# Performance work log

Hardware: AMD Instinct MI355X
Metric: run time of the kernel (lower is better)

Reference implementation:

```python
import jax, jax.numpy as jnp
import numpy as np

N = 50000      # nodes
E = 800000     # edges (before self-loops)
IN = 256       # in_channels
HID = 64       # hidden_channels per head
HEADS = 8
OUT = 64       # out_channels
NEG_SLOPE = 0.2  # PyG GATConv leaky_relu slope


def gat_conv(x, W, a_src, a_dst, b, src, dst, heads, outc, concat):
    # x: [n, f_in]; W: [f_in, heads*outc]; a_src/a_dst: [heads, outc]; b: bias
    n = x.shape[0]
    h = (x @ W).reshape(n, heads, outc)                      # [n, H, C]
    alpha_s = (h * a_src).sum(-1)                            # [n, H]
    alpha_d = (h * a_dst).sum(-1)                            # [n, H]
    e = jax.nn.leaky_relu(alpha_s[src] + alpha_d[dst], NEG_SLOPE)  # [E, H]
    # segment softmax over destination node
    m = jax.lax.stop_gradient(jax.ops.segment_max(e, dst, num_segments=n))
    ex = jnp.exp(e - m[dst])                                 # [E, H]
    den = jax.ops.segment_sum(ex, dst, num_segments=n)       # [n, H]
    alpha = ex / (den[dst] + 1e-16)                          # [E, H]
    out = jax.ops.segment_sum(alpha[..., None] * h[src], dst, num_segments=n)  # [n, H, C]
    out = out.reshape(n, heads * outc) if concat else out.mean(axis=1)
    return out + b


def setup_inputs() -> dict:
    key = jax.random.key(0)
    ks = jax.random.split(key, 10)
    s = 0.1
    return {
        "x": jax.random.normal(ks[0], (N, IN), jnp.float32),
        "edge_index": jax.random.randint(ks[1], (2, E), 0, N, dtype=jnp.int64)
            if jax.config.jax_enable_x64 else jax.random.randint(ks[1], (2, E), 0, N, dtype=jnp.int32),
        "W1": jax.random.normal(ks[2], (IN, HEADS * HID), jnp.float32) * s,
        "a_src1": jax.random.normal(ks[3], (HEADS, HID), jnp.float32) * s,
        "a_dst1": jax.random.normal(ks[4], (HEADS, HID), jnp.float32) * s,
        "b1": jnp.zeros((HEADS * HID,), jnp.float32),
        "W2": jax.random.normal(ks[5], (HEADS * HID, OUT), jnp.float32) * s,
        "a_src2": jax.random.normal(ks[6], (1, OUT), jnp.float32) * s,
        "a_dst2": jax.random.normal(ks[7], (1, OUT), jnp.float32) * s,
        "b2": jnp.zeros((OUT,), jnp.float32),
    }


def reference(x, W1, a_src1, a_dst1, b1, W2, a_src2, a_dst2, b2, edge_index):
    # eval mode: dropout is identity. PyG GATConv adds self-loops by default.
    loop = jnp.arange(N, dtype=edge_index.dtype)
    src = jnp.concatenate([edge_index[0], loop])
    dst = jnp.concatenate([edge_index[1], loop])
    h = jax.nn.elu(gat_conv(x, W1, a_src1, a_dst1, b1, src, dst, HEADS, HID, True))
    return gat_conv(h, W2, a_src2, a_dst2, b2, src, dst, 1, OUT, False)
```

## Files before the change

### kernel.cpp

```cpp
#include <hip/hip_runtime.h>
#include <cstddef>

#define NN   50000
#define EE   800000
#define TOTE 850000
#define INC  256
#define HEADS 8
#define F1   512
#define OUTC 64
#define NB   ((NN + 255) / 256)

#define PB_CVTX   ((NN * INC / 8 + 255) / 256)
#define PB_CVTW1  ((INC * F1 + 255) / 256)
#define PB_CVTW2  ((F1 * OUTC + 255) / 256)
#define PB_COUNT  ((TOTE + 255) / 256)

typedef unsigned short ushort_t;
typedef unsigned int uint_t;
typedef __attribute__((ext_vector_type(8))) short short8;
typedef __attribute__((ext_vector_type(4))) float f32x4;

__device__ __forceinline__ ushort_t f32_to_bf16_rne(float f) {
  uint_t u = __float_as_uint(f);
  u += 0x7fffu + ((u >> 16) & 1u);
  return (ushort_t)(u >> 16);
}
__device__ __forceinline__ float bf16lo_to_f32(uint_t u) {
  return __uint_as_float(u << 16);
}
__device__ __forceinline__ float bf16hi_to_f32(uint_t u) {
  return __uint_as_float(u & 0xffff0000u);
}
__device__ __forceinline__ float lrelu(float x) { return fmaxf(x, 0.2f * x); }

__device__ __forceinline__ void gload16(const ushort_t* g, ushort_t* l) {
  __builtin_amdgcn_global_load_lds(
      (const __attribute__((address_space(1))) void*)g,
      (__attribute__((address_space(3))) void*)l, 16, 0, 0);
}

__global__ __launch_bounds__(256)
void prelude_kernel(const float* __restrict__ x, ushort_t* __restrict__ xbf,
                    const float* __restrict__ W1, ushort_t* __restrict__ W1T,
                    const float* __restrict__ W2, ushort_t* __restrict__ W2T,
                    const int* __restrict__ dsts, int* __restrict__ deg) {
  int b = blockIdx.x;
  if (b < PB_CVTX) {
    long i = ((long)b * 256 + threadIdx.x) * 8;
    if (i >= (long)NN * INC) return;
    float4 v0 = *reinterpret_cast<const float4*>(x + i);
    float4 v1 = *reinterpret_cast<const float4*>(x + i + 4);
    ushort_t p[8] = {f32_to_bf16_rne(v0.x), f32_to_bf16_rne(v0.y),
                     f32_to_bf16_rne(v0.z), f32_to_bf16_rne(v0.w),
                     f32_to_bf16_rne(v1.x), f32_to_bf16_rne(v1.y),
                     f32_to_bf16_rne(v1.z), f32_to_bf16_rne(v1.w)};
    *reinterpret_cast<uint4*>(xbf + i) = *reinterpret_cast<uint4*>(p);
    return;
  }
  b -= PB_CVTX;
  if (b < PB_CVTW1) {
    int i = b * 256 + threadIdx.x;
    if (i >= INC * F1) return;
    int k = i / F1, n = i % F1;
    W1T[(size_t)n * INC + k] = f32_to_bf16_rne(W1[i]);
    return;
  }
  b -= PB_CVTW1;
  if (b < PB_CVTW2) {
    int i = b * 256 + threadIdx.x;
    if (i >= F1 * OUTC) return;
    int k = i / OUTC, n = i % OUTC;
    W2T[(size_t)n * F1 + k] = f32_to_bf16_rne(W2[i]);
    return;
  }
  b -= PB_CVTW2;
  {
    int e = b * 256 + threadIdx.x;
    if (e >= TOTE) return;
    int dst = (e < EE) ? dsts[e] : (e - EE);
    atomicAdd(&deg[dst], 1);
  }
}

__global__ __launch_bounds__(256, 2)
void gemm_mfma(const ushort_t* __restrict__ A, const ushort_t* __restrict__ BT,
               const float* __restrict__ a_src, const float* __restrict__ a_dst,
               ushort_t* __restrict__ Cbf, float* __restrict__ AS,
               float* __restrict__ AD, int M, int K, int Nn, int nheads) {
  __shared__ __align__(16) ushort_t sA[128 * 64];
  __shared__ __align__(16) ushort_t sB[64 * 64];
  const int tid = threadIdx.x;
  const int w = tid >> 6, lane = tid & 63;

  int p = blockIdx.x;
  int nwg = gridDim.x;
  int l = ((nwg & 7) == 0) ? ((p & 7) * (nwg >> 3) + (p >> 3)) : p;
  const int rowBase = (l / nheads) * 128;
  const int head = l % nheads;
  const int colBase = head * 64;

  const int l8 = lane >> 3;
  const int srcslot = (lane & 7) ^ l8;
  size_t aOff[4]; ushort_t* aLds[4];
  #pragma unroll
  for (int q = 0; q < 4; ++q) {
    int r0 = w * 32 + q * 8;
    int grow = rowBase + r0 + l8; if (grow > M - 1) grow = M - 1;
    aOff[q] = (size_t)grow * K + srcslot * 8;
    aLds[q] = sA + r0 * 64;
  }
  size_t bOff[2]; ushort_t* bLds[2];
  #pragma unroll
  for (int q = 0; q < 2; ++q) {
    int c0 = w * 16 + q * 8;
    bOff[q] = (size_t)(colBase + c0 + l8) * K + srcslot * 8;
    bLds[q] = sB + c0 * 64;
  }

  f32x4 acc[2][4];
  #pragma unroll
  for (int mf = 0; mf < 2; ++mf)
    #pragma unroll
    for (int cf = 0; cf < 4; ++cf)
      acc[mf][cf] = (f32x4){0.f, 0.f, 0.f, 0.f};

  const int nkt = K >> 6;
  for (int kt = 0; kt < nkt; ++kt) {
    __syncthreads();
    #pragma unroll
    for (int q = 0; q < 4; ++q) gload16(A + aOff[q] + kt * 64, aLds[q]);
    #pragma unroll
    for (int q = 0; q < 2; ++q) gload16(BT + bOff[q] + kt * 64, bLds[q]);
    __syncthreads();
    #pragma unroll
    for (int ks = 0; ks < 2; ++ks) {
      const int sl = ks * 4 + (lane >> 4);
      short8 af[2], bfr[4];
      #pragma unroll
      for (int mf = 0; mf < 2; ++mf) {
        int row = w * 32 + mf * 16 + (lane & 15);
        af[mf] = *reinterpret_cast<short8*>((char*)sA + row * 128 + ((sl ^ (row & 7)) << 4));
      }
      #pragma unroll
      for (int cf = 0; cf < 4; ++cf) {
        int col = cf * 16 + (lane & 15);
        bfr[cf] = *reinterpret_cast<short8*>((char*)sB + col * 128 + ((sl ^ (col & 7)) << 4));
      }
      #pragma unroll
      for (int mf = 0; mf < 2; ++mf)
        #pragma unroll
        for (int cf = 0; cf < 4; ++cf)
          acc[mf][cf] = __builtin_amdgcn_mfma_f32_16x16x32_bf16(af[mf], bfr[cf], acc[mf][cf], 0, 0, 0);
    }
  }

  const int g = lane >> 4, c = lane & 15;
  float asv[4], adv[4];
  #pragma unroll
  for (int cf = 0; cf < 4; ++cf) {
    asv[cf] = a_src[colBase + cf * 16 + c];
    adv[cf] = a_dst[colBase + cf * 16 + c];
  }
  #pragma unroll
  for (int mf = 0; mf < 2; ++mf) {
    #pragma unroll
    for (int r = 0; r < 4; ++r) {
      int row = rowBase + w * 32 + mf * 16 + g * 4 + r;
      bool ok = row < M;
      float s = 0.f, d = 0.f;
      #pragma unroll
      for (int cf = 0; cf < 4; ++cf) {
        float v = acc[mf][cf][r];
        s = fmaf(v, asv[cf], s);
        d = fmaf(v, adv[cf], d);
        if (ok) Cbf[(size_t)row * Nn + colBase + cf * 16 + c] = f32_to_bf16_rne(v);
      }
      #pragma unroll
      for (int off = 8; off > 0; off >>= 1) {
        s += __shfl_xor(s, off);
        d += __shfl_xor(d, off);
      }
      if (ok && c == 0) {
        AS[(size_t)row * nheads + head] = s;
        AD[(size_t)row * nheads + head] = d;
      }
    }
  }
}

__global__ __launch_bounds__(256)
void scanA_kernel(const int* __restrict__ deg, int* __restrict__ rowptr,
                  int* __restrict__ psum) {
  __shared__ int sh[256];
  int t = threadIdx.x;
  int i = blockIdx.x * 256 + t;
  int v = (i < NN) ? deg[i] : 0;
  sh[t] = v;
  __syncthreads();
  #pragma unroll
  for (int off = 1; off < 256; off <<= 1) {
    int t2 = (t >= off) ? sh[t - off] : 0;
    __syncthreads();
    sh[t] += t2;
    __syncthreads();
  }
  if (i < NN) rowptr[i + 1] = sh[t];
  if (t == 255) psum[blockIdx.x] = sh[255];
}

__global__ __launch_bounds__(256)
void scanC_kernel(int* __restrict__ rowptr, const int* __restrict__ psum) {
  __shared__ int sh[256];
  int t = threadIdx.x;
  int v = (t < NB) ? psum[t] : 0;
  sh[t] = v;
  __syncthreads();
  #pragma unroll
  for (int off = 1; off < 256; off <<= 1) {
    int t2 = (t >= off) ? sh[t - off] : 0;
    __syncthreads();
    sh[t] += t2;
    __syncthreads();
  }
  int base = (blockIdx.x > 0) ? sh[blockIdx.x - 1] : 0;
  int i = blockIdx.x * 256 + t;
  if (i < NN) rowptr[i + 1] += base;
  if (i == 0) rowptr[0] = 0;
}

__global__ __launch_bounds__(256)
void scatter_kernel(const int* __restrict__ srcs, const int* __restrict__ dsts,
                    const int* __restrict__ rowptr, int* __restrict__ cursor,
                    int* __restrict__ esrc) {
  int e = blockIdx.x * blockDim.x + threadIdx.x;
  if (e >= TOTE) return;
  int src, dst;
  if (e < EE) { src = srcs[e]; dst = dsts[e]; }
  else        { src = e - EE;  dst = e - EE; }
  int pos = rowptr[dst] + atomicAdd(&cursor[dst], 1);
  esrc[pos] = src;
}

__global__ __launch_bounds__(256)
void agg1_kernel(const ushort_t* __restrict__ H1bf, const float* __restrict__ AS,
                 const float* __restrict__ AD, const int* __restrict__ rowptr,
                 const int* __restrict__ esrc, const float* __restrict__ b1,
                 ushort_t* __restrict__ OUT) {
  int n = (blockIdx.x * blockDim.x + threadIdx.x) >> 6;
  int lane = threadIdx.x & 63;
  if (n >= NN) return;
  int off = lane * 8;
  int h = lane >> 3;
  float ad = AD[n * HEADS + h];
  int s0 = rowptr[n], s1 = rowptr[n + 1];
  float den = 0.f;
  float a0 = 0.f, a1 = 0.f, a2 = 0.f, a3 = 0.f, a4 = 0.f, a5 = 0.f, a6 = 0.f, a7 = 0.f;
  int j = s0;
  for (; j + 3 < s1; j += 4) {
    int src[4];
    #pragma unroll
    for (int u = 0; u < 4; ++u) src[u] = esrc[j + u];
    float as[4]; uint4 v[4];
    #pragma unroll
    for (int u = 0; u < 4; ++u) {
      as[u] = AS[src[u] * HEADS + h];
      v[u] = *reinterpret_cast<const uint4*>(H1bf + (size_t)src[u] * F1 + off);
    }
    #pragma unroll
    for (int u = 0; u < 4; ++u) {
      float wgt = __expf(lrelu(as[u] + ad));
      den += wgt;
      a0 = fmaf(wgt, bf16lo_to_f32(v[u].x), a0);
      a1 = fmaf(wgt, bf16hi_to_f32(v[u].x), a1);
      a2 = fmaf(wgt, bf16lo_to_f32(v[u].y), a2);
      a3 = fmaf(wgt, bf16hi_to_f32(v[u].y), a3);
      a4 = fmaf(wgt, bf16lo_to_f32(v[u].z), a4);
      a5 = fmaf(wgt, bf16hi_to_f32(v[u].z), a5);
      a6 = fmaf(wgt, bf16lo_to_f32(v[u].w), a6);
      a7 = fmaf(wgt, bf16hi_to_f32(v[u].w), a7);
    }
  }
  for (; j < s1; ++j) {
    int src = esrc[j];
    float as = AS[src * HEADS + h];
    uint4 v = *reinterpret_cast<const uint4*>(H1bf + (size_t)src * F1 + off);
    float wgt = __expf(lrelu(as + ad));
    den += wgt;
    a0 = fmaf(wgt, bf16lo_to_f32(v.x), a0);
    a1 = fmaf(wgt, bf16hi_to_f32(v.x), a1);
    a2 = fmaf(wgt, bf16lo_to_f32(v.y), a2);
    a3 = fmaf(wgt, bf16hi_to_f32(v.y), a3);
    a4 = fmaf(wgt, bf16lo_to_f32(v.z), a4);
    a5 = fmaf(wgt, bf16hi_to_f32(v.z), a5);
    a6 = fmaf(wgt, bf16lo_to_f32(v.w), a6);
    a7 = fmaf(wgt, bf16hi_to_f32(v.w), a7);
  }
  float rden = 1.f / (den + 1e-16f);
  float4 b_lo = *reinterpret_cast<const float4*>(b1 + off);
  float4 b_hi = *reinterpret_cast<const float4*>(b1 + off + 4);
  float r[8];
  r[0] = fmaf(a0, rden, b_lo.x); r[1] = fmaf(a1, rden, b_lo.y);
  r[2] = fmaf(a2, rden, b_lo.z); r[3] = fmaf(a3, rden, b_lo.w);
  r[4] = fmaf(a4, rden, b_hi.x); r[5] = fmaf(a5, rden, b_hi.y);
  r[6] = fmaf(a6, rden, b_hi.z); r[7] = fmaf(a7, rden, b_hi.w);
  ushort_t pk[8];
  #pragma unroll
  for (int i = 0; i < 8; ++i) {
    float e = r[i] > 0.f ? r[i] : expm1f(r[i]);
    pk[i] = f32_to_bf16_rne(e);
  }
  *reinterpret_cast<uint4*>(OUT + (size_t)n * F1 + off) = *reinterpret_cast<uint4*>(pk);
}

__global__ __launch_bounds__(256)
void agg2_kernel(const ushort_t* __restrict__ H2bf, const float* __restrict__ AS,
                 const float* __restrict__ AD, const int* __restrict__ rowptr,
                 const int* __restrict__ esrc, const float* __restrict__ b2,
                 float* __restrict__ OUT) {
  int n = (blockIdx.x * blockDim.x + threadIdx.x) >> 6;
  int lane = threadIdx.x & 63;
  if (n >= NN) return;
  int grp = lane >> 3;
  int c8 = (lane & 7) * 8;
  float ad = AD[n];
  int s0 = rowptr[n], s1 = rowptr[n + 1];
  float den = 0.f;
  float a0 = 0.f, a1 = 0.f, a2 = 0.f, a3 = 0.f, a4 = 0.f, a5 = 0.f, a6 = 0.f, a7 = 0.f;
  for (int j0 = s0; j0 < s1; j0 += 8) {
    int j = j0 + grp;
    bool valid = j < s1;
    int src = esrc[valid ? j : s0];
    float as = AS[src];
    uint4 v = *reinterpret_cast<const uint4*>(H2bf + (size_t)src * OUTC + c8);
    float w = valid ? __expf(lrelu(as + ad)) : 0.f;
    den += w;
    a0 = fmaf(w, bf16lo_to_f32(v.x), a0);
    a1 = fmaf(w, bf16hi_to_f32(v.x), a1);
    a2 = fmaf(w, bf16lo_to_f32(v.y), a2);
    a3 = fmaf(w, bf16hi_to_f32(v.y), a3);
    a4 = fmaf(w, bf16lo_to_f32(v.z), a4);
    a5 = fmaf(w, bf16hi_to_f32(v.z), a5);
    a6 = fmaf(w, bf16lo_to_f32(v.w), a6);
    a7 = fmaf(w, bf16hi_to_f32(v.w), a7);
  }
  #pragma unroll
  for (int st = 8; st < 64; st <<= 1) {
    den += __shfl_xor(den, st);
    a0 += __shfl_xor(a0, st); a1 += __shfl_xor(a1, st);
    a2 += __shfl_xor(a2, st); a3 += __shfl_xor(a3, st);
    a4 += __shfl_xor(a4, st); a5 += __shfl_xor(a5, st);
    a6 += __shfl_xor(a6, st); a7 += __shfl_xor(a7, st);
  }
  if (grp == 0) {
    float rden = 1.f / (den + 1e-16f);
    float4 o0, o1;
    o0.x = fmaf(a0, rden, b2[c8 + 0]); o0.y = fmaf(a1, rden, b2[c8 + 1]);
    o0.z = fmaf(a2, rden, b2[c8 + 2]); o0.w = fmaf(a3, rden, b2[c8 + 3]);
    o1.x = fmaf(a4, rden, b2[c8 + 4]); o1.y = fmaf(a5, rden, b2[c8 + 5]);
    o1.z = fmaf(a6, rden, b2[c8 + 6]); o1.w = fmaf(a7, rden, b2[c8 + 7]);
    *reinterpret_cast<float4*>(OUT + (size_t)n * OUTC + c8) = o0;
    *reinterpret_cast<float4*>(OUT + (size_t)n * OUTC + c8 + 4) = o1;
  }
}

extern "C" void kernel_launch(void* const* d_in, const int* in_sizes, int n_in,
                              void* d_out, int out_size, void* d_ws, size_t ws_size,
                              hipStream_t stream) {
  const float* x      = (const float*)d_in[0];
  const int*   edges  = (const int*)d_in[1];
  const float* W1     = (const float*)d_in[2];
  const float* a_src1 = (const float*)d_in[3];
  const float* a_dst1 = (const float*)d_in[4];
  const float* b1     = (const float*)d_in[5];
  const float* W2     = (const float*)d_in[6];
  const float* a_src2 = (const float*)d_in[7];
  const float* a_dst2 = (const float*)d_in[8];
  const float* b2     = (const float*)d_in[9];
  float* out = (float*)d_out;

  const int* srcs = edges;
  const int* dsts = edges + EE;

  float* AS1    = (float*)d_ws;
  float* AD1    = AS1    + (size_t)NN * HEADS;
  float* AS2    = AD1    + (size_t)NN * HEADS;
  float* AD2    = AS2    + NN;
  ushort_t* xbf   = (ushort_t*)(AD2 + NN);
  ushort_t* W1T   = xbf  + (size_t)NN * INC;
  ushort_t* W2T   = W1T  + (size_t)F1 * INC;
  ushort_t* H1bf  = W2T  + (size_t)OUTC * F1;
  ushort_t* AG1bf = H1bf + (size_t)NN * F1;
  ushort_t* H2bf  = AG1bf + (size_t)NN * F1;
  int* deg    = (int*)(H2bf + (size_t)NN * OUTC);
  int* rowptr = deg + NN;
  int* cursor = rowptr + NN + 1;
  int* psum   = cursor + NN;
  int* esrc   = psum + NB;

  hipMemsetAsync(deg, 0, (size_t)(3 * NN + 1) * sizeof(int), stream);

  prelude_kernel<<<PB_CVTX + PB_CVTW1 + PB_CVTW2 + PB_COUNT, 256, 0, stream>>>(
      x, xbf, W1, W1T, W2, W2T, dsts, deg);

  scanA_kernel<<<NB, 256, 0, stream>>>(deg, rowptr, psum);
  scanC_kernel<<<NB, 256, 0, stream>>>(rowptr, psum);
  scatter_kernel<<<(TOTE + 255) / 256, 256, 0, stream>>>(srcs, dsts, rowptr, cursor, esrc);

  gemm_mfma<<<((NN + 127) / 128) * HEADS, 256, 0, stream>>>(
      xbf, W1T, a_src1, a_dst1, H1bf, AS1, AD1, NN, INC, F1, HEADS);
  agg1_kernel<<<(NN * 64 + 255) / 256, 256, 0, stream>>>(H1bf, AS1, AD1, rowptr, esrc, b1, AG1bf);

  gemm_mfma<<<(NN + 127) / 128, 256, 0, stream>>>(
      AG1bf, W2T, a_src2, a_dst2, H2bf, AS2, AD2, NN, F1, OUTC, 1);
  agg2_kernel<<<(NN * 64 + 255) / 256, 256, 0, stream>>>(H2bf, AS2, AD2, rowptr, esrc, b2, out);
}
```

Before: 312.1 us.

## Split layer-1 aggregation per head and process eight edges per wavefront

The layer-1 aggregation now gives each wavefront one (node, head) pair instead of one whole node. The wavefront's 8 lane groups each take a different incoming edge, and a cross-group shuffle reduction merges the partial sums. The attention score arrays written by the GEMM epilogue move from node-major to head-major, so per-head score reads are contiguous. The aim is more parallel gathers in flight and shorter serial dependency chains per wavefront. The cost is 8x more wavefronts, repeated edge-index loads for each head, shuffle overhead, and only one lane group doing the final store.

After: 391.9 us. 25.6% more time.

```diff
diff --git a/kernel.cpp b/kernel.cpp
--- a/kernel.cpp
+++ b/kernel.cpp
@@ -181,8 +181,8 @@
         d += __shfl_xor(d, off);
       }
       if (ok && c == 0) {
-        AS[(size_t)row * nheads + head] = s;
-        AD[(size_t)row * nheads + head] = d;
+        AS[(size_t)head * M + row] = s;
+        AD[(size_t)head * M + row] = d;
       }
     }
   }
@@ -246,70 +246,57 @@
                  const float* __restrict__ AD, const int* __restrict__ rowptr,
                  const int* __restrict__ esrc, const float* __restrict__ b1,
                  ushort_t* __restrict__ OUT) {
-  int n = (blockIdx.x * blockDim.x + threadIdx.x) >> 6;
-  int lane = threadIdx.x & 63;
+  const int h = blockIdx.x & 7;
+  const int n = (blockIdx.x >> 3) * 4 + (threadIdx.x >> 6);
+  const int lane = threadIdx.x & 63;
   if (n >= NN) return;
-  int off = lane * 8;
-  int h = lane >> 3;
-  float ad = AD[n * HEADS + h];
+  const int grp = lane >> 3;
+  const int slot = lane & 7;
+  const int ch = h * 64 + slot * 8;
+  float ad = AD[(size_t)h * NN + n];
   int s0 = rowptr[n], s1 = rowptr[n + 1];
   float den = 0.f;
   float a0 = 0.f, a1 = 0.f, a2 = 0.f, a3 = 0.f, a4 = 0.f, a5 = 0.f, a6 = 0.f, a7 = 0.f;
-  int j = s0;
-  for (; j + 3 < s1; j += 4) {
-    int src[4];
-    #pragma unroll
-    for (int u = 0; u < 4; ++u) src[u] = esrc[j + u];
-    float as[4]; uint4 v[4];
-    #pragma unroll
-    for (int u = 0; u < 4; ++u) {
-      as[u] = AS[src[u] * HEADS + h];
-      v[u] = *reinterpret_cast<const uint4*>(H1bf + (size_t)src[u] * F1 + off);
+  for (int j0 = s0; j0 < s1; j0 += 8) {
+    int j = j0 + grp;
+    bool valid = j < s1;
+    int src = esrc[valid ? j : s0];
+    float as = AS[(size_t)h * NN + src];
+    uint4 v = *reinterpret_cast<const uint4*>(H1bf + (size_t)src * F1 + ch);
+    float w = valid ? __expf(lrelu(as + ad)) : 0.f;
+    den += w;
+    a0 = fmaf(w, bf16lo_to_f32(v.x), a0);
+    a1 = fmaf(w, bf16hi_to_f32(v.x), a1);
+    a2 = fmaf(w, bf16lo_to_f32(v.y), a2);
+    a3 = fmaf(w, bf16hi_to_f32(v.y), a3);
+    a4 = fmaf(w, bf16lo_to_f32(v.z), a4);
+    a5 = fmaf(w, bf16hi_to_f32(v.z), a5);
+    a6 = fmaf(w, bf16lo_to_f32(v.w), a6);
+    a7 = fmaf(w, bf16hi_to_f32(v.w), a7);
+  }
+  #pragma unroll
+  for (int st = 8; st < 64; st <<= 1) {
+    den += __shfl_xor(den, st);
+    a0 += __shfl_xor(a0, st); a1 += __shfl_xor(a1, st);
+    a2 += __shfl_xor(a2, st); a3 += __shfl_xor(a3, st);
+    a4 += __shfl_xor(a4, st); a5 += __shfl_xor(a5, st);
+    a6 += __shfl_xor(a6, st); a7 += __shfl_xor(a7, st);
+  }
+  if (grp == 0) {
+    float rden = 1.f / (den + 1e-16f);
+    float r[8];
+    r[0] = fmaf(a0, rden, b1[ch + 0]); r[1] = fmaf(a1, rden, b1[ch + 1]);
+    r[2] = fmaf(a2, rden, b1[ch + 2]); r[3] = fmaf(a3, rden, b1[ch + 3]);
+    r[4] = fmaf(a4, rden, b1[ch + 4]); r[5] = fmaf(a5, rden, b1[ch + 5]);
+    r[6] = fmaf(a6, rden, b1[ch + 6]); r[7] = fmaf(a7, rden, b1[ch + 7]);
+    ushort_t pk[8];
+    #pragma unroll
+    for (int i = 0; i < 8; ++i) {
+      float e = r[i] > 0.f ? r[i] : expm1f(r[i]);
+      pk[i] = f32_to_bf16_rne(e);
     }
-    #pragma unroll
-    for (int u = 0; u < 4; ++u) {
-      float wgt = __expf(lrelu(as[u] + ad));
-      den += wgt;
-      a0 = fmaf(wgt, bf16lo_to_f32(v[u].x), a0);
-      a1 = fmaf(wgt, bf16hi_to_f32(v[u].x), a1);
-      a2 = fmaf(wgt, bf16lo_to_f32(v[u].y), a2);
-      a3 = fmaf(wgt, bf16hi_to_f32(v[u].y), a3);
-      a4 = fmaf(wgt, bf16lo_to_f32(v[u].z), a4);
-      a5 = fmaf(wgt, bf16hi_to_f32(v[u].z), a5);
-      a6 = fmaf(wgt, bf16lo_to_f32(v[u].w), a6);
-      a7 = fmaf(wgt, bf16hi_to_f32(v[u].w), a7);
-    }
-  }
-  for (; j < s1; ++j) {
-    int src = esrc[j];
-    float as = AS[src * HEADS + h];
-    uint4 v = *reinterpret_cast<const uint4*>(H1bf + (size_t)src * F1 + off);
-    float wgt = __expf(lrelu(as + ad));
-    den += wgt;
-    a0 = fmaf(wgt, bf16lo_to_f32(v.x), a0);
-    a1 = fmaf(wgt, bf16hi_to_f32(v.x), a1);
-    a2 = fmaf(wgt, bf16lo_to_f32(v.y), a2);
-    a3 = fmaf(wgt, bf16hi_to_f32(v.y), a3);
-    a4 = fmaf(wgt, bf16lo_to_f32(v.z), a4);
-    a5 = fmaf(wgt, bf16hi_to_f32(v.z), a5);
-    a6 = fmaf(wgt, bf16lo_to_f32(v.w), a6);
-    a7 = fmaf(wgt, bf16hi_to_f32(v.w), a7);
-  }
-  float rden = 1.f / (den + 1e-16f);
-  float4 b_lo = *reinterpret_cast<const float4*>(b1 + off);
-  float4 b_hi = *reinterpret_cast<const float4*>(b1 + off + 4);
-  float r[8];
-  r[0] = fmaf(a0, rden, b_lo.x); r[1] = fmaf(a1, rden, b_lo.y);
-  r[2] = fmaf(a2, rden, b_lo.z); r[3] = fmaf(a3, rden, b_lo.w);
-  r[4] = fmaf(a4, rden, b_hi.x); r[5] = fmaf(a5, rden, b_hi.y);
-  r[6] = fmaf(a6, rden, b_hi.z); r[7] = fmaf(a7, rden, b_hi.w);
-  ushort_t pk[8];
-  #pragma unroll
-  for (int i = 0; i < 8; ++i) {
-    float e = r[i] > 0.f ? r[i] : expm1f(r[i]);
-    pk[i] = f32_to_bf16_rne(e);
-  }
-  *reinterpret_cast<uint4*>(OUT + (size_t)n * F1 + off) = *reinterpret_cast<uint4*>(pk);
+    *reinterpret_cast<uint4*>(OUT + (size_t)n * F1 + ch) = *reinterpret_cast<uint4*>(pk);
+  }
 }
 
 __global__ __launch_bounds__(256)
@@ -408,7 +395,7 @@
 
   gemm_mfma<<<((NN + 127) / 128) * HEADS, 256, 0, stream>>>(
       xbf, W1T, a_src1, a_dst1, H1bf, AS1, AD1, NN, INC, F1, HEADS);
-  agg1_kernel<<<(NN * 64 + 255) / 256, 256, 0, stream>>>(H1bf, AS1, AD1, rowptr, esrc, b1, AG1bf);
+  agg1_kernel<<<((NN + 3) / 4) * 8, 256, 0, stream>>>(H1bf, AS1, AD1, rowptr, esrc, b1, AG1bf);
 
   gemm_mfma<<<(NN + 127) / 128, 256, 0, stream>>>(
       AG1bf, W2T, a_src2, a_dst2, H2bf, AS2, AD2, NN, F1, OUTC, 1);
```
